# Kernel optimization log

Measured on AMD Instinct MI355X. Metric: run time of the kernel, lower is better.

Reference implementation:

```python
import jax, jax.numpy as jnp
import numpy as np

EPS = 1e-6  # flax LayerNorm default

def _layer_norm(x, scale, bias):
    mu = jnp.mean(x, axis=-1, keepdims=True)
    var = jnp.mean(jnp.square(x - mu), axis=-1, keepdims=True)
    return (x - mu) * jax.lax.rsqrt(var + EPS) * scale + bias

def setup_inputs() -> dict:
    key = jax.random.key(0)
    ks = jax.random.split(key, 8)
    B, S, D_in, D_h, D_out, N = 4, 2048, 1024, 2048, 1024, 6
    init = lambda k, shape, fan_in: jax.random.normal(k, shape, jnp.float32) / np.sqrt(fan_in)
    return {
        "x": jax.random.normal(ks[0], (B, S, D_in), jnp.float32),
        "ln1_scale": jnp.ones((D_in,), jnp.float32),
        "ln1_bias": jnp.zeros((D_in,), jnp.float32),
        "w1": init(ks[1], (D_in, D_h), D_in),
        "b1": jnp.zeros((D_h,), jnp.float32),
        "block_ln_scales": jnp.ones((N, D_h), jnp.float32),
        "block_ln_biases": jnp.zeros((N, D_h), jnp.float32),
        "block_ws": init(ks[2], (N, D_h, D_h), D_h),
        "block_bs": jnp.zeros((N, D_h), jnp.float32),
        "ln2_scale": jnp.ones((D_h,), jnp.float32),
        "ln2_bias": jnp.zeros((D_h,), jnp.float32),
        "w2": init(ks[3], (D_h, D_out), D_h),
        "b2": jnp.zeros((D_out,), jnp.float32),
    }

def reference(x, ln1_scale, ln1_bias, w1, b1, block_ln_scales, block_ln_biases,
              block_ws, block_bs, ln2_scale, ln2_bias, w2, b2):
    # stem: LN -> Linear -> SiLU
    h = _layer_norm(x, ln1_scale, ln1_bias)
    h = jax.nn.silu(jnp.einsum('bsd,dh->bsh', h, w1) + b1)

    # residual blocks via scan over stacked params
    def block(h, params):
        s, b, w, lb = params
        y = _layer_norm(h, s, b)
        y = jax.nn.silu(jnp.einsum('bsh,hk->bsk', y, w) + lb)
        return h + y, None

    h, _ = jax.lax.scan(block, h, (block_ln_scales, block_ln_biases, block_ws, block_bs))

    # head: LN -> Linear
    h = _layer_norm(h, ln2_scale, ln2_bias)
    return jnp.einsum('bsh,ho->bso', h, w2) + b2
```

## Files before the change

### kernel.cpp

```cpp
#include <hip/hip_runtime.h>
#include <hip/hip_bf16.h>

typedef short short8 __attribute__((ext_vector_type(8)));
typedef float f32x4 __attribute__((ext_vector_type(4)));

#define AS1(p) ((const __attribute__((address_space(1))) void*)(p))
#define AS3(p) ((__attribute__((address_space(3))) void*)(p))

__device__ __forceinline__ ushort f2bf(float f) {
  __hip_bfloat16 h = __float2bfloat16(f);
  return *reinterpret_cast<const ushort*>(&h);
}
__device__ __forceinline__ float bfu2f(ushort u) {
  unsigned int x = ((unsigned int)u) << 16;
  float f;
  __builtin_memcpy(&f, &x, 4);
  return f;
}
__device__ __forceinline__ float silu_f(float v) { return v / (1.f + __expf(-v)); }

template<int NV>
__global__ __launch_bounds__(256) void ln_bf16_k(
    const float* __restrict__ in, const float* __restrict__ sc,
    const float* __restrict__ bi, ushort* __restrict__ out)
{
  const int D = NV * 1024;
  const long row = blockIdx.x;
  const int tx = threadIdx.x;
  const float* p = in + row * (long)D;
  float4 v[NV];
  float s = 0.f, s2 = 0.f;
#pragma unroll
  for (int t = 0; t < NV; ++t) {
    v[t] = *reinterpret_cast<const float4*>(p + t * 1024 + tx * 4);
    s  += v[t].x + v[t].y + v[t].z + v[t].w;
    s2 += v[t].x * v[t].x + v[t].y * v[t].y + v[t].z * v[t].z + v[t].w * v[t].w;
  }
#pragma unroll
  for (int o = 1; o < 64; o <<= 1) { s += __shfl_xor(s, o); s2 += __shfl_xor(s2, o); }
  __shared__ float red[2][4];
  const int wave = tx >> 6;
  if ((tx & 63) == 0) { red[0][wave] = s; red[1][wave] = s2; }
  __syncthreads();
  s  = red[0][0] + red[0][1] + red[0][2] + red[0][3];
  s2 = red[1][0] + red[1][1] + red[1][2] + red[1][3];
  const float mu   = s / D;
  const float rstd = rsqrtf(s2 / D - mu * mu + 1e-6f);
#pragma unroll
  for (int t = 0; t < NV; ++t) {
    const int d = t * 1024 + tx * 4;
    float4 g = *reinterpret_cast<const float4*>(sc + d);
    float4 b = *reinterpret_cast<const float4*>(bi + d);
    ushort4 o;
    o.x = f2bf((v[t].x - mu) * rstd * g.x + b.x);
    o.y = f2bf((v[t].y - mu) * rstd * g.y + b.y);
    o.z = f2bf((v[t].z - mu) * rstd * g.z + b.z);
    o.w = f2bf((v[t].w - mu) * rstd * g.w + b.w);
    *reinterpret_cast<ushort4*>(out + row * (long)D + d) = o;
  }
}

__global__ __launch_bounds__(256) void ln_bf16b_k(
    const ushort* __restrict__ in, const float* __restrict__ sc,
    const float* __restrict__ bi, ushort* __restrict__ out)
{
  const long row = blockIdx.x;
  const int tx = threadIdx.x;
  const int d = tx * 8;
  short8 v8 = *reinterpret_cast<const short8*>(in + row * 2048 + d);
  float v[8];
  float s = 0.f, s2 = 0.f;
#pragma unroll
  for (int j = 0; j < 8; ++j) {
    v[j] = bfu2f((ushort)v8[j]);
    s += v[j]; s2 += v[j] * v[j];
  }
#pragma unroll
  for (int o = 1; o < 64; o <<= 1) { s += __shfl_xor(s, o); s2 += __shfl_xor(s2, o); }
  __shared__ float red[2][4];
  const int wave = tx >> 6;
  if ((tx & 63) == 0) { red[0][wave] = s; red[1][wave] = s2; }
  __syncthreads();
  s  = red[0][0] + red[0][1] + red[0][2] + red[0][3];
  s2 = red[1][0] + red[1][1] + red[1][2] + red[1][3];
  const float mu   = s * (1.f / 2048.f);
  const float rstd = rsqrtf(s2 * (1.f / 2048.f) - mu * mu + 1e-6f);
  float4 g0 = *reinterpret_cast<const float4*>(sc + d);
  float4 g1 = *reinterpret_cast<const float4*>(sc + d + 4);
  float4 b0 = *reinterpret_cast<const float4*>(bi + d);
  float4 b1 = *reinterpret_cast<const float4*>(bi + d + 4);
  const float gg[8] = {g0.x, g0.y, g0.z, g0.w, g1.x, g1.y, g1.z, g1.w};
  const float bb[8] = {b0.x, b0.y, b0.z, b0.w, b1.x, b1.y, b1.z, b1.w};
  short8 o8;
#pragma unroll
  for (int j = 0; j < 8; ++j)
    o8[j] = (short)f2bf((v[j] - mu) * rstd * gg[j] + bb[j]);
  *reinterpret_cast<short8*>(out + row * 2048 + d) = o8;
}

__global__ __launch_bounds__(256) void transpose_bf16_k(
    const float* __restrict__ in, ushort* __restrict__ out, int K, int N)
{
  __shared__ float tile[64][65];
  const int k0 = blockIdx.y * 64, n0 = blockIdx.x * 64;
  const int tx = threadIdx.x, ty = threadIdx.y;
#pragma unroll
  for (int r = ty; r < 64; r += 4)
    tile[r][tx] = in[(long)(k0 + r) * N + n0 + tx];
  __syncthreads();
#pragma unroll
  for (int r = ty; r < 64; r += 4)
    out[(long)(n0 + r) * K + k0 + tx] = f2bf(tile[tx][r]);
}

#define STG(gsrc, ldst)                                                          \
  __builtin_amdgcn_global_load_lds(AS1(gsrc),          AS3(ldst),        16, 0, 0); \
  __builtin_amdgcn_global_load_lds(AS1((gsrc) + offQ), AS3((ldst) + 8192), 16, 0, 0);

#define ldsA(B, H) (ldsW + (B) * 65536 + (H) * 16384)
#define ldsB(B, H) (ldsW + (B) * 65536 + 32768 + (H) * 16384)

#define LOAD_A(dst, DB, ihalf)                                                  \
  _Pragma("unroll") for (int i_ = 0; i_ < 4; ++i_) {                            \
    dst[i_][0] = *(const short8*)(smem + (DB) * 65536 + aOff + ((ihalf) * 4 + i_) * 2048 + rdk0); \
    dst[i_][1] = *(const short8*)(smem + (DB) * 65536 + aOff + ((ihalf) * 4 + i_) * 2048 + rdk1); \
  }

#define LOAD_B(dst, DB, jhalf)                                                  \
  _Pragma("unroll") for (int j_ = 0; j_ < 2; ++j_) {                            \
    dst[j_][0] = *(const short8*)(smem + (DB) * 65536 + bOff + ((jhalf) * 2 + j_) * 2048 + rdk0); \
    dst[j_][1] = *(const short8*)(smem + (DB) * 65536 + bOff + ((jhalf) * 2 + j_) * 2048 + rdk1); \
  }

#define MFMA_Q(ihalf, jhalf, afr, bfr)                                          \
  __builtin_amdgcn_s_setprio(1);                                                \
  _Pragma("unroll") for (int kk_ = 0; kk_ < 2; ++kk_)                           \
  _Pragma("unroll") for (int i_ = 0; i_ < 4; ++i_)                              \
  _Pragma("unroll") for (int j_ = 0; j_ < 2; ++j_)                              \
    acc[(ihalf) * 4 + i_][(jhalf) * 2 + j_] =                                   \
        __builtin_amdgcn_mfma_f32_16x16x32_bf16(afr[i_][kk_], bfr[j_][kk_],     \
            acc[(ihalf) * 4 + i_][(jhalf) * 2 + j_], 0, 0, 0);                  \
  __builtin_amdgcn_s_setprio(0);

#define DO_TILE(CUR, NXT, BA, BB, AO1, AO2, BO2, S0, S2, S3, TAILW, PFB)        \
  LOAD_A(af, CUR, 0);                                                           \
  if (S0) { STG(aP + (AO1) + offH, ldsA(NXT, 1)); }                             \
  __builtin_amdgcn_s_barrier();                                                 \
  MFMA_Q(0, 0, af, BA);                                                         \
  MFMA_Q(0, 1, af, BB);                                                         \
  __builtin_amdgcn_s_barrier();                                                 \
  LOAD_A(af, CUR, 1);                                                           \
  if (S2) { STG(bP + (BO2), ldsB(CUR, 0)); }                                    \
  __builtin_amdgcn_s_barrier();                                                 \
  MFMA_Q(1, 1, af, BB);                                                         \
  __builtin_amdgcn_s_barrier();                                                 \
  if (S3) { STG(bP + (BO2) + offH, ldsB(CUR, 1)); STG(aP + (AO2), ldsA(CUR, 0)); } \
  if (S3)            { asm volatile("s_waitcnt vmcnt(6)" ::: "memory"); }       \
  else if (TAILW)    { asm volatile("s_waitcnt vmcnt(0)" ::: "memory"); }       \
  __builtin_amdgcn_sched_barrier(0);                                            \
  __builtin_amdgcn_s_barrier();                                                 \
  MFMA_Q(1, 0, af, BA);                                                         \
  if (PFB) { LOAD_B(BB, NXT, 0); LOAD_B(BA, NXT, 1); }                          \
  __builtin_amdgcn_s_barrier();

template<int MODE>
__global__ __launch_bounds__(512, 2) void gemm256_k(
    const ushort* __restrict__ A, const ushort* __restrict__ Bt,
    const float* __restrict__ bias, void* __restrict__ Cv,
    int M, int N, int K)
{
  extern __shared__ char smem[];
  const int tid = threadIdx.x;
  const int lane = tid & 63, wid = tid >> 6;
  const int wr = wid >> 2, wc = wid & 3;
  const int nbx = N >> 8;

  int bid;
  {
    const int b = blockIdx.x;
    const int cpx = gridDim.x >> 3;
    bid = (b & 7) * cpx + (b >> 3);
  }
  const int bx = bid % nbx, by = bid / nbx;
  const long m0 = (long)by << 8, n0 = (long)bx << 8;

  const int srow = tid >> 3;
  const int scol = (((tid & 7) * 16) ^ (((tid >> 3) & 7) << 4)) >> 1;
  const ushort* aP = A  + (m0 + srow) * (long)K + scol;
  const ushort* bP = Bt + (n0 + srow) * (long)K + scol;
  const long offH = 128L * K, offQ = 64L * K;
  char* ldsW = smem + wid * 1024;

  const int rdk0 = (((lane >> 4) * 16)     ) ^ ((lane & 7) << 4);
  const int rdk1 = (((lane >> 4) * 16) + 64) ^ ((lane & 7) << 4);
  const int aOff = wr * 16384 + (lane & 15) * 128;
  const int bOff = 32768 + (wc >> 1) * 16384 + ((wc & 1) * 64 + (lane & 15)) * 128;

  f32x4 acc[8][4] = {};
  const int NT = K >> 6;

  STG(aP,           ldsA(0, 0));  STG(aP + offH,      ldsA(0, 1));
  STG(bP,           ldsB(0, 0));  STG(bP + offH,      ldsB(0, 1));
  STG(bP + 64,      ldsB(1, 0));  STG(bP + 64 + offH, ldsB(1, 1));
  STG(aP + 64,      ldsA(1, 0));
  asm volatile("s_waitcnt vmcnt(6)" ::: "memory");
  __builtin_amdgcn_sched_barrier(0);
  __builtin_amdgcn_s_barrier();

  short8 af[4][2], bfA[2][2], bfB[2][2];
  LOAD_B(bfA, 0, 0);
  LOAD_B(bfB, 0, 1);

  for (int t = 0; t < NT - 2; t += 2) {
    DO_TILE(0, 1, bfA, bfB,  64, 128, 128, 1, 1, 1, 0, 1)
    DO_TILE(1, 0, bfB, bfA, 128, 192, 192, 1, 1, 1, 0, 1)
    aP += 128; bP += 128;
  }
  DO_TILE(0, 1, bfA, bfB, 64, 0, 0, 1, 0, 0, 1, 1)
  DO_TILE(1, 0, bfB, bfA,  0, 0, 0, 0, 0, 0, 0, 0)

#pragma unroll
  for (int j = 0; j < 4; ++j) {
    const long col = n0 + wc * 64 + j * 16 + (lane & 15);
    const float bj = bias[col];
#pragma unroll
    for (int i = 0; i < 8; ++i) {
      const long rowb = m0 + wr * 128 + i * 16 + ((lane >> 4) << 2);
#pragma unroll
      for (int r = 0; r < 4; ++r) {
        const float v = acc[i][j][r] + bj;
        const long idx = (rowb + r) * N + col;
        if (MODE == 0) {
          ((ushort*)Cv)[idx] = f2bf(silu_f(v));
        } else if (MODE == 1) {
          ushort* C = (ushort*)Cv;
          C[idx] = f2bf(bfu2f(C[idx]) + silu_f(v));
        } else {
          ((float*)Cv)[idx] = v;
        }
      }
    }
  }
}

extern "C" void kernel_launch(void* const* d_in, const int* in_sizes, int n_in,
                              void* d_out, int out_size, void* d_ws, size_t ws_size,
                              hipStream_t stream) {
  const float* x     = (const float*)d_in[0];
  const float* ln1_s = (const float*)d_in[1];
  const float* ln1_b = (const float*)d_in[2];
  const float* w1    = (const float*)d_in[3];
  const float* b1    = (const float*)d_in[4];
  const float* bln_s = (const float*)d_in[5];
  const float* bln_b = (const float*)d_in[6];
  const float* bws   = (const float*)d_in[7];
  const float* bbs   = (const float*)d_in[8];
  const float* ln2_s = (const float*)d_in[9];
  const float* ln2_b = (const float*)d_in[10];
  const float* w2    = (const float*)d_in[11];
  const float* b2    = (const float*)d_in[12];
  float* out = (float*)d_out;

  const int M = 8192;
  char* ws = (char*)d_ws;
  ushort* h   = (ushort*)ws;
  ushort* Abf = (ushort*)(ws + 33554432);
  ushort* wt  = (ushort*)(ws + 67108864);
  const long W1T = 0;
  const long BLK = 2097152;
  const long W2T = BLK + 6L * 4194304;

  (void)hipFuncSetAttribute((const void*)gemm256_k<0>,
      hipFuncAttributeMaxDynamicSharedMemorySize, 131072);
  (void)hipFuncSetAttribute((const void*)gemm256_k<1>,
      hipFuncAttributeMaxDynamicSharedMemorySize, 131072);
  (void)hipFuncSetAttribute((const void*)gemm256_k<2>,
      hipFuncAttributeMaxDynamicSharedMemorySize, 131072);

  dim3 tb(64, 4);
  transpose_bf16_k<<<dim3(2048 / 64, 1024 / 64), tb, 0, stream>>>(w1, wt + W1T, 1024, 2048);
  for (int i = 0; i < 6; ++i)
    transpose_bf16_k<<<dim3(32, 32), tb, 0, stream>>>(
        bws + (long)i * 2048 * 2048, wt + BLK + (long)i * 4194304, 2048, 2048);
  transpose_bf16_k<<<dim3(1024 / 64, 2048 / 64), tb, 0, stream>>>(w2, wt + W2T, 2048, 1024);

  ln_bf16_k<1><<<M, 256, 0, stream>>>(x, ln1_s, ln1_b, Abf);
  gemm256_k<0><<<32 * 8, 512, 131072, stream>>>(Abf, wt + W1T, b1, (void*)h, M, 2048, 1024);

  for (int i = 0; i < 6; ++i) {
    ln_bf16b_k<<<M, 256, 0, stream>>>(h, bln_s + i * 2048, bln_b + i * 2048, Abf);
    gemm256_k<1><<<32 * 8, 512, 131072, stream>>>(
        Abf, wt + BLK + (long)i * 4194304, bbs + i * 2048, (void*)h, M, 2048, 2048);
  }

  ln_bf16b_k<<<M, 256, 0, stream>>>(h, ln2_s, ln2_b, Abf);
  gemm256_k<2><<<32 * 4, 512, 131072, stream>>>(Abf, wt + W2T, b2, (void*)out, M, 1024, 2048);
}
```

Measured before the change: 755.8 us.

## Restructure GEMM main loop into four k-split MFMA phases with reordered LDS staging

Reworks the 256x256 bf16 GEMM inner tile schedule. Each K tile is now split into four 16-MFMA phases, one per (M-half, K-subslice) pair. Each phase holds only one A fragment set and per-K-slice B fragments, with explicit lgkmcnt waits and barriers between phases. The global-to-LDS staging order also changes: both A halves of the next buffer are issued at the start and B loads are spread across phases, with a vmcnt(4) wait at tile end. The goal is fewer live fragment registers and better overlap of LDS reads, global prefetch and MFMA work. The cost is more barriers and lgkmcnt(0) stalls per tile.

```diff
diff --git a/kernel.cpp b/kernel.cpp
--- a/kernel.cpp
+++ b/kernel.cpp
@@ -114,54 +114,59 @@
 }
 
 #define STG(gsrc, ldst)                                                          \
-  __builtin_amdgcn_global_load_lds(AS1(gsrc),          AS3(ldst),        16, 0, 0); \
-  __builtin_amdgcn_global_load_lds(AS1((gsrc) + offQ), AS3((ldst) + 8192), 16, 0, 0);
+  __builtin_amdgcn_global_load_lds(AS1(gsrc),          AS3(ldst),          16, 0, 0); \
+  __builtin_amdgcn_global_load_lds(AS1((gsrc) + offQ), AS3((ldst) + 8192), 16, 0, 0)
 
 #define ldsA(B, H) (ldsW + (B) * 65536 + (H) * 16384)
 #define ldsB(B, H) (ldsW + (B) * 65536 + 32768 + (H) * 16384)
 
-#define LOAD_A(dst, DB, ihalf)                                                  \
-  _Pragma("unroll") for (int i_ = 0; i_ < 4; ++i_) {                            \
-    dst[i_][0] = *(const short8*)(smem + (DB) * 65536 + aOff + ((ihalf) * 4 + i_) * 2048 + rdk0); \
-    dst[i_][1] = *(const short8*)(smem + (DB) * 65536 + aOff + ((ihalf) * 4 + i_) * 2048 + rdk1); \
-  }
-
-#define LOAD_B(dst, DB, jhalf)                                                  \
-  _Pragma("unroll") for (int j_ = 0; j_ < 2; ++j_) {                            \
-    dst[j_][0] = *(const short8*)(smem + (DB) * 65536 + bOff + ((jhalf) * 2 + j_) * 2048 + rdk0); \
-    dst[j_][1] = *(const short8*)(smem + (DB) * 65536 + bOff + ((jhalf) * 2 + j_) * 2048 + rdk1); \
-  }
-
-#define MFMA_Q(ihalf, jhalf, afr, bfr)                                          \
-  __builtin_amdgcn_s_setprio(1);                                                \
-  _Pragma("unroll") for (int kk_ = 0; kk_ < 2; ++kk_)                           \
+#define RD_AF(DB, MH, KS)                                                       \
   _Pragma("unroll") for (int i_ = 0; i_ < 4; ++i_)                              \
-  _Pragma("unroll") for (int j_ = 0; j_ < 2; ++j_)                              \
-    acc[(ihalf) * 4 + i_][(jhalf) * 2 + j_] =                                   \
-        __builtin_amdgcn_mfma_f32_16x16x32_bf16(afr[i_][kk_], bfr[j_][kk_],     \
-            acc[(ihalf) * 4 + i_][(jhalf) * 2 + j_], 0, 0, 0);                  \
-  __builtin_amdgcn_s_setprio(0);
-
-#define DO_TILE(CUR, NXT, BA, BB, AO1, AO2, BO2, S0, S2, S3, TAILW, PFB)        \
-  LOAD_A(af, CUR, 0);                                                           \
-  if (S0) { STG(aP + (AO1) + offH, ldsA(NXT, 1)); }                             \
-  __builtin_amdgcn_s_barrier();                                                 \
-  MFMA_Q(0, 0, af, BA);                                                         \
-  MFMA_Q(0, 1, af, BB);                                                         \
-  __builtin_amdgcn_s_barrier();                                                 \
-  LOAD_A(af, CUR, 1);                                                           \
-  if (S2) { STG(bP + (BO2), ldsB(CUR, 0)); }                                    \
-  __builtin_amdgcn_s_barrier();                                                 \
-  MFMA_Q(1, 1, af, BB);                                                         \
-  __builtin_amdgcn_s_barrier();                                                 \
-  if (S3) { STG(bP + (BO2) + offH, ldsB(CUR, 1)); STG(aP + (AO2), ldsA(CUR, 0)); } \
-  if (S3)            { asm volatile("s_waitcnt vmcnt(6)" ::: "memory"); }       \
-  else if (TAILW)    { asm volatile("s_waitcnt vmcnt(0)" ::: "memory"); }       \
-  __builtin_amdgcn_sched_barrier(0);                                            \
-  __builtin_amdgcn_s_barrier();                                                 \
-  MFMA_Q(1, 0, af, BA);                                                         \
-  if (PFB) { LOAD_B(BB, NXT, 0); LOAD_B(BA, NXT, 1); }                          \
-  __builtin_amdgcn_s_barrier();
+    af[i_] = *(const short8*)(smem + (DB) * 65536 + aOff + ((MH) * 4 + i_) * 2048 + rdk[(KS)])
+
+#define RD_BF(DST, DB, KS)                                                      \
+  _Pragma("unroll") for (int j_ = 0; j_ < 4; ++j_)                              \
+    DST[j_] = *(const short8*)(smem + (DB) * 65536 + bOff + j_ * 2048 + rdk[(KS)])
+
+#define MFMA16(MH, BFR)                                                         \
+  _Pragma("unroll") for (int i_ = 0; i_ < 4; ++i_)                              \
+  _Pragma("unroll") for (int j_ = 0; j_ < 4; ++j_)                              \
+    acc[(MH) * 4 + i_][j_] = __builtin_amdgcn_mfma_f32_16x16x32_bf16(           \
+        af[i_], BFR[j_], acc[(MH) * 4 + i_][j_], 0, 0, 0)
+
+#define BARRIER __builtin_amdgcn_s_barrier()
+#define LGKM0 do { asm volatile("s_waitcnt lgkmcnt(0)");                        \
+                   __builtin_amdgcn_sched_barrier(0); } while (0)
+#define W4 do { asm volatile("s_waitcnt vmcnt(4)" ::: "memory");                \
+                __builtin_amdgcn_sched_barrier(0); } while (0)
+#define W0 do { asm volatile("s_waitcnt vmcnt(0)" ::: "memory");                \
+                __builtin_amdgcn_sched_barrier(0); } while (0)
+#define WN do {} while (0)
+
+#define DO_TILE(DB, S1, AO, S2, BO, WAITE)                                      \
+  RD_AF(DB, 0, 0);                                                              \
+  RD_BF(bf0, DB, 0);                                                            \
+  RD_BF(bf1, DB, 1);                                                            \
+  if (S1) { STG(aP + (AO), ldsA((DB) ^ 1, 0));                                  \
+            STG(aP + (AO) + offH, ldsA((DB) ^ 1, 1)); }                         \
+  BARRIER; LGKM0;                                                               \
+  __builtin_amdgcn_s_setprio(1); MFMA16(0, bf0); __builtin_amdgcn_s_setprio(0); \
+  BARRIER;                                                                      \
+  RD_AF(DB, 1, 0);                                                              \
+  if (S2) { STG(bP + (BO), ldsB(DB, 0)); }                                      \
+  BARRIER; LGKM0;                                                               \
+  __builtin_amdgcn_s_setprio(1); MFMA16(1, bf0); __builtin_amdgcn_s_setprio(0); \
+  BARRIER;                                                                      \
+  RD_AF(DB, 0, 1);                                                              \
+  if (S2) { STG(bP + (BO) + offH, ldsB(DB, 1)); }                               \
+  BARRIER; LGKM0;                                                               \
+  __builtin_amdgcn_s_setprio(1); MFMA16(0, bf1); __builtin_amdgcn_s_setprio(0); \
+  BARRIER;                                                                      \
+  RD_AF(DB, 1, 1);                                                              \
+  BARRIER; LGKM0;                                                               \
+  __builtin_amdgcn_s_setprio(1); MFMA16(1, bf1); __builtin_amdgcn_s_setprio(0); \
+  WAITE;                                                                        \
+  BARRIER;
 
 template<int MODE>
 __global__ __launch_bounds__(512, 2) void gemm256_k(
@@ -191,33 +196,29 @@
   const long offH = 128L * K, offQ = 64L * K;
   char* ldsW = smem + wid * 1024;
 
-  const int rdk0 = (((lane >> 4) * 16)     ) ^ ((lane & 7) << 4);
-  const int rdk1 = (((lane >> 4) * 16) + 64) ^ ((lane & 7) << 4);
+  int rdk[2];
+  rdk[0] = (((lane >> 4) * 16)     ) ^ ((lane & 7) << 4);
+  rdk[1] = (((lane >> 4) * 16) + 64) ^ ((lane & 7) << 4);
   const int aOff = wr * 16384 + (lane & 15) * 128;
   const int bOff = 32768 + (wc >> 1) * 16384 + ((wc & 1) * 64 + (lane & 15)) * 128;
 
   f32x4 acc[8][4] = {};
   const int NT = K >> 6;
 
-  STG(aP,           ldsA(0, 0));  STG(aP + offH,      ldsA(0, 1));
-  STG(bP,           ldsB(0, 0));  STG(bP + offH,      ldsB(0, 1));
-  STG(bP + 64,      ldsB(1, 0));  STG(bP + 64 + offH, ldsB(1, 1));
-  STG(aP + 64,      ldsA(1, 0));
-  asm volatile("s_waitcnt vmcnt(6)" ::: "memory");
-  __builtin_amdgcn_sched_barrier(0);
-  __builtin_amdgcn_s_barrier();
-
-  short8 af[4][2], bfA[2][2], bfB[2][2];
-  LOAD_B(bfA, 0, 0);
-  LOAD_B(bfB, 0, 1);
-
+  STG(aP,      ldsA(0, 0));  STG(aP + offH,      ldsA(0, 1));
+  STG(bP,      ldsB(0, 0));  STG(bP + offH,      ldsB(0, 1));
+  STG(bP + 64, ldsB(1, 0));  STG(bP + 64 + offH, ldsB(1, 1));
+  W4;
+  BARRIER;
+
+  short8 af[4], bf0[4], bf1[4];
   for (int t = 0; t < NT - 2; t += 2) {
-    DO_TILE(0, 1, bfA, bfB,  64, 128, 128, 1, 1, 1, 0, 1)
-    DO_TILE(1, 0, bfB, bfA, 128, 192, 192, 1, 1, 1, 0, 1)
+    DO_TILE(0, 1,  64, 1, 128, W4)
+    DO_TILE(1, 1, 128, 1, 192, W4)
     aP += 128; bP += 128;
   }
-  DO_TILE(0, 1, bfA, bfB, 64, 0, 0, 1, 0, 0, 1, 1)
-  DO_TILE(1, 0, bfB, bfA,  0, 0, 0, 0, 0, 0, 0, 0)
+  DO_TILE(0, 1, 64, 0, 0, W0)
+  DO_TILE(1, 0,  0, 0, 0, WN)
 
 #pragma unroll
   for (int j = 0; j < 4; ++j) {
```

Result: no change. 759.8 us (+0.5%).
